# Optimization experiments

Measured on AMD Instinct MI355X. Metric: run time of the kernel, lower is better.

The kernel has to match this reference:

```python
import jax, jax.numpy as jnp
import numpy as np

EMB = 384
H = 6
D = 64  # head_size = EMB // H
FF = 4 * EMB
B, T = 256, 256
EPS = 1e-5


def layernorm(x, g, b):
    mu = jnp.mean(x, axis=-1, keepdims=True)
    var = jnp.var(x, axis=-1, keepdims=True)
    return (x - mu) * jax.lax.rsqrt(var + EPS) * g + b


def setup_inputs() -> dict:
    key = jax.random.key(0)
    ks = jax.random.split(key, 12)
    s_qkv = 1.0 / np.sqrt(EMB)
    return {
        "x":  jax.random.normal(ks[0], (B, T, EMB), jnp.float32),
        # per-head Q/K/V projections stacked: [EMB, H, D]
        "Wq": jax.random.normal(ks[1], (EMB, H, D), jnp.float32) * s_qkv,
        "Wk": jax.random.normal(ks[2], (EMB, H, D), jnp.float32) * s_qkv,
        "Wv": jax.random.normal(ks[3], (EMB, H, D), jnp.float32) * s_qkv,
        "Wo": jax.random.normal(ks[4], (EMB, EMB), jnp.float32) * s_qkv,
        "bo": jnp.zeros((EMB,), jnp.float32),
        "W1": jax.random.normal(ks[5], (EMB, FF), jnp.float32) * s_qkv,
        "b1": jnp.zeros((FF,), jnp.float32),
        "W2": jax.random.normal(ks[6], (FF, EMB), jnp.float32) * (1.0 / np.sqrt(FF)),
        "b2": jnp.zeros((EMB,), jnp.float32),
        "g1": jnp.ones((EMB,), jnp.float32),
        "be1": jnp.zeros((EMB,), jnp.float32),
        "g2": jnp.ones((EMB,), jnp.float32),
        "be2": jnp.zeros((EMB,), jnp.float32),
    }


def reference(x, Wq, Wk, Wv, Wo, bo, W1, b1, W2, b2, g1, be1, g2, be2):
    # pre-LN attention (unmasked encoder block, dropout in eval mode = identity)
    h = layernorm(x, g1, be1)                      # [B,T,C]
    q = jnp.einsum('btc,chd->bhtd', h, Wq)
    k = jnp.einsum('btc,chd->bhtd', h, Wk)
    v = jnp.einsum('btc,chd->bhtd', h, Wv)
    scores = jnp.einsum('bhtd,bhsd->bhts', q, k) * (D ** -0.5)
    attn = jax.nn.softmax(scores, axis=-1)         # [B,H,T,T]
    o = jnp.einsum('bhts,bhsd->bhtd', attn, v)
    o = o.transpose(0, 2, 1, 3).reshape(x.shape[0], x.shape[1], EMB)  # concat heads
    x = x + o @ Wo + bo
    h2 = layernorm(x, g2, be2)
    ff = jax.nn.relu(h2 @ W1 + b1) @ W2 + b2
    return x + ff
```

## Files before the change

### kernel.cpp

```cpp
#include <hip/hip_runtime.h>

typedef __attribute__((ext_vector_type(8))) short bf16x8;
typedef __attribute__((ext_vector_type(4))) float f32x4;
typedef __attribute__((ext_vector_type(4))) unsigned short u16x4;

#define DEVFN static __device__ __forceinline__

DEVFN unsigned short f2b(float f) {
  union { float f; unsigned u; } x; x.f = f;
  unsigned r = x.u + 0x7FFFu + ((x.u >> 16) & 1u);
  return (unsigned short)(r >> 16);
}

DEVFN void gll16(const void* g, void* l) {
  __builtin_amdgcn_global_load_lds(
      (const __attribute__((address_space(1))) unsigned int*)g,
      (__attribute__((address_space(3))) unsigned int*)l, 16, 0, 0);
}

#define MFMA16(a, b, c) __builtin_amdgcn_mfma_f32_16x16x32_bf16((a), (b), (c), 0, 0, 0)

__global__ __launch_bounds__(256) void prep_kernel(
    const float* __restrict__ Wq, const float* __restrict__ Wk, const float* __restrict__ Wv,
    const float* __restrict__ Wo, const float* __restrict__ W1, const float* __restrict__ W2,
    short* __restrict__ wqkvT, short* __restrict__ woT,
    short* __restrict__ w1T, short* __restrict__ w2T)
{
  int idx = blockIdx.x * 256 + threadIdx.x;
  if (idx < 442368) {
    int n = idx / 384, kk = idx - n * 384;
    int sec = n / 384, ww = n - sec * 384;
    const float* s = sec == 0 ? Wq : (sec == 1 ? Wk : Wv);
    wqkvT[idx] = (short)f2b(s[kk * 384 + ww]);
  } else if (idx < 589824) {
    int j = idx - 442368;
    int n = j / 384, kk = j - n * 384;
    woT[j] = (short)f2b(Wo[kk * 384 + n]);
  } else if (idx < 1179648) {
    int j = idx - 589824;
    int n = j / 384, kk = j - n * 384;
    w1T[j] = (short)f2b(W1[kk * 1536 + n]);
  } else if (idx < 1769472) {
    int j = idx - 1179648;
    int n = j / 1536, kk = j - n * 1536;
    w2T[j] = (short)f2b(W2[kk * 384 + n]);
  }
}

__global__ __launch_bounds__(256) void ln_kernel(
    const float* __restrict__ x, const float* __restrict__ g, const float* __restrict__ b,
    short* __restrict__ out)
{
  int row = blockIdx.x * 4 + (threadIdx.x >> 6);
  int l = threadIdx.x & 63;
  const float* xr = x + (size_t)row * 384;
  float v[6], s = 0.f, s2 = 0.f;
  #pragma unroll
  for (int i = 0; i < 6; ++i) { v[i] = xr[l + 64 * i]; s += v[i]; s2 += v[i] * v[i]; }
  #pragma unroll
  for (int m = 1; m < 64; m <<= 1) { s += __shfl_xor(s, m); s2 += __shfl_xor(s2, m); }
  float mu = s * (1.f / 384.f);
  float rs = rsqrtf(s2 * (1.f / 384.f) - mu * mu + 1e-5f);
  short* orow = out + (size_t)row * 384;
  #pragma unroll
  for (int i = 0; i < 6; ++i) {
    int c = l + 64 * i;
    orow[c] = (short)f2b((v[i] - mu) * rs * g[c] + b[c]);
  }
}

template<int EPI>
__global__ __launch_bounds__(512) void gemm_bt(
    const short* __restrict__ A, const short* __restrict__ BT,
    int K, int kt, int N, int nx,
    const float* __restrict__ bias, const float* __restrict__ resid,
    float* __restrict__ fout, short* __restrict__ bout,
    short* __restrict__ qb, short* __restrict__ kb, short* __restrict__ vb)
{
  __shared__ short As[256 * 64];
  __shared__ short Bs[128 * 64];
  const int tid = threadIdx.x;
  const int l = tid & 63, w = tid >> 6;
  const int cl = l & 15, rq = l >> 4;
  const int wr = (w >> 1) * 64, wc = (w & 1) * 64;

  const int nwg = gridDim.x, bid = blockIdx.x;
  const int q8 = nwg >> 3, r8 = nwg & 7;
  const int xcd = bid & 7, ii = bid >> 3;
  const int wg = (xcd < r8) ? xcd * (q8 + 1) + ii : r8 * (q8 + 1) + (xcd - r8) * q8 + ii;
  const int bx = wg % nx, by = wg / nx;

  const int m0 = by * 256, n0 = bx * 128;
  const short* Ab = A + (size_t)m0 * K;
  const short* Bb = BT + (size_t)n0 * K;

  f32x4 acc[4][4] = {};

  for (int ks = 0; ks < kt; ++ks) {
    const int k0 = ks * 64;
    __syncthreads();
    #pragma unroll
    for (int i = 0; i < 4; ++i) {
      int slot = i * 512 + tid;
      int row = slot >> 3, g = slot & 7;
      int gs = g ^ (row & 7);
      gll16(Ab + (size_t)row * K + k0 + gs * 8, &As[slot * 8]);
    }
    #pragma unroll
    for (int i = 0; i < 2; ++i) {
      int slot = i * 512 + tid;
      int row = slot >> 3, g = slot & 7;
      int gs = g ^ (row & 7);
      gll16(Bb + (size_t)row * K + k0 + gs * 8, &Bs[slot * 8]);
    }
    __syncthreads();
    #pragma unroll
    for (int kk = 0; kk < 2; ++kk) {
      bf16x8 af[4], bfr[4];
      #pragma unroll
      for (int m = 0; m < 4; ++m) {
        int row = wr + m * 16 + cl;
        af[m] = *(const bf16x8*)&As[row * 64 + (((kk * 4 + rq) ^ (row & 7)) * 8)];
      }
      #pragma unroll
      for (int n = 0; n < 4; ++n) {
        int row = wc + n * 16 + cl;
        bfr[n] = *(const bf16x8*)&Bs[row * 64 + (((kk * 4 + rq) ^ (row & 7)) * 8)];
      }
      #pragma unroll
      for (int m = 0; m < 4; ++m)
        #pragma unroll
        for (int n = 0; n < 4; ++n)
          acc[m][n] = MFMA16(af[m], bfr[n], acc[m][n]);
    }
  }

  const int gr0 = m0 + wr, gc0 = n0 + wc;
  #pragma unroll
  for (int m = 0; m < 4; ++m) {
    #pragma unroll
    for (int n = 0; n < 4; ++n) {
      int col = gc0 + n * 16 + cl;
      int rbase = gr0 + m * 16 + rq * 4;
      if constexpr (EPI == 0) {
        int sec = col / 384;
        int wcol = col - sec * 384;
        int hh = wcol >> 6, d = wcol & 63;
        int bidx = rbase >> 8, t0 = rbase & 255;
        if (sec == 2) {
          u16x4 pk;
          #pragma unroll
          for (int r = 0; r < 4; ++r) pk[r] = f2b(acc[m][n][r]);
          *(u16x4*)&vb[((size_t)(bidx * 6 + hh) * 64 + d) * 256 + t0] = pk;
        } else {
          short* dst = (sec == 0) ? qb : kb;
          float sc = (sec == 0) ? 0.125f : 1.0f;
          #pragma unroll
          for (int r = 0; r < 4; ++r)
            dst[((size_t)(bidx * 6 + hh) * 256 + t0 + r) * 64 + d] = (short)f2b(acc[m][n][r] * sc);
        }
      } else if constexpr (EPI == 1) {
        #pragma unroll
        for (int r = 0; r < 4; ++r) {
          size_t ix = (size_t)(rbase + r) * N + col;
          fout[ix] = acc[m][n][r] + bias[col] + resid[ix];
        }
      } else {
        #pragma unroll
        for (int r = 0; r < 4; ++r)
          bout[(size_t)(rbase + r) * N + col] = (short)f2b(fmaxf(acc[m][n][r] + bias[col], 0.f));
      }
    }
  }
}

__global__ __launch_bounds__(256) void attn_kernel(
    const short* __restrict__ qg, const short* __restrict__ kg,
    const short* __restrict__ vg, short* __restrict__ og)
{
  __shared__ short Ks[256 * 64];
  __shared__ short Vs[64 * 256];
  __shared__ float Pb[4][16 * 36];
  const int tid = threadIdx.x;
  const int bh = blockIdx.x >> 2;
  const int q0 = (blockIdx.x & 3) * 64;
  const int w = tid >> 6, l = tid & 63;
  const int cl = l & 15, rq = l >> 4;
  const short* kgb = kg + (size_t)bh * 16384;
  const short* vgb = vg + (size_t)bh * 16384;
  #pragma unroll
  for (int i = 0; i < 8; ++i) {
    int slot = i * 256 + tid;
    int row = slot >> 3, g = slot & 7;
    gll16(kgb + row * 64 + (g ^ (row & 7)) * 8, &Ks[slot * 8]);
  }
  #pragma unroll
  for (int i = 0; i < 8; ++i) {
    int slot = i * 256 + tid;
    int row = slot >> 5, g = slot & 31;
    int gs = (g & 24) | ((g ^ row) & 7);
    gll16(vgb + row * 256 + gs * 8, &Vs[slot * 8]);
  }
  const int qrow = q0 + w * 16 + cl;
  const bf16x8* qp = (const bf16x8*)(qg + ((size_t)bh * 256 + qrow) * 64 + rq * 8);
  bf16x8 qf0 = qp[0];
  bf16x8 qf1 = qp[4];
  __syncthreads();

  f32x4 s[16] = {};
  #pragma unroll
  for (int c = 0; c < 16; ++c) {
    int scol = c * 16 + cl;
    bf16x8 b0 = *(const bf16x8*)&Ks[scol * 64 + ((rq ^ (scol & 7)) * 8)];
    bf16x8 b1 = *(const bf16x8*)&Ks[scol * 64 + (((4 + rq) ^ (scol & 7)) * 8)];
    s[c] = MFMA16(qf0, b0, s[c]);
    s[c] = MFMA16(qf1, b1, s[c]);
  }
  float mx[4], inv[4];
  #pragma unroll
  for (int r = 0; r < 4; ++r) {
    float m = s[0][r];
    #pragma unroll
    for (int c = 1; c < 16; ++c) m = fmaxf(m, s[c][r]);
    #pragma unroll
    for (int msk = 1; msk < 16; msk <<= 1) m = fmaxf(m, __shfl_xor(m, msk));
    mx[r] = m;
  }
  #pragma unroll
  for (int r = 0; r < 4; ++r) {
    float t = 0.f;
    #pragma unroll
    for (int c = 0; c < 16; ++c) { float e = __expf(s[c][r] - mx[r]); s[c][r] = e; t += e; }
    #pragma unroll
    for (int msk = 1; msk < 16; msk <<= 1) t += __shfl_xor(t, msk);
    inv[r] = 1.f / t;
  }
  #pragma unroll
  for (int c = 0; c < 16; ++c) {
    #pragma unroll
    for (int r = 0; r < 4; ++r) s[c][r] *= inv[r];
  }
  f32x4 oacc[4] = {};
  float* Pw = Pb[w];
  #pragma unroll
  for (int ch = 0; ch < 8; ++ch) {
    #pragma unroll
    for (int r = 0; r < 4; ++r) {
      Pw[(4 * rq + r) * 36 + cl]      = s[2 * ch][r];
      Pw[(4 * rq + r) * 36 + 16 + cl] = s[2 * ch + 1][r];
    }
    f32x4 lo = *(const f32x4*)&Pw[cl * 36 + rq * 8];
    f32x4 hi = *(const f32x4*)&Pw[cl * 36 + rq * 8 + 4];
    bf16x8 pa;
    #pragma unroll
    for (int j = 0; j < 4; ++j) { pa[j] = (short)f2b(lo[j]); pa[j + 4] = (short)f2b(hi[j]); }
    #pragma unroll
    for (int n = 0; n < 4; ++n) {
      int vrow = n * 16 + cl;
      int gg = ch * 4 + rq;
      int gs = (gg & 24) | ((gg ^ vrow) & 7);
      bf16x8 vf = *(const bf16x8*)&Vs[vrow * 256 + gs * 8];
      oacc[n] = MFMA16(pa, vf, oacc[n]);
    }
  }
  int b = bh / 6, hh = bh - b * 6;
  #pragma unroll
  for (int n = 0; n < 4; ++n) {
    #pragma unroll
    for (int r = 0; r < 4; ++r) {
      int trow = q0 + w * 16 + 4 * rq + r;
      og[((size_t)(b * 256 + trow)) * 384 + hh * 64 + n * 16 + cl] = (short)f2b(oacc[n][r]);
    }
  }
}

extern "C" void kernel_launch(void* const* d_in, const int* in_sizes, int n_in,
                              void* d_out, int out_size, void* d_ws, size_t ws_size,
                              hipStream_t stream) {
  const float* x   = (const float*)d_in[0];
  const float* Wq  = (const float*)d_in[1];
  const float* Wk  = (const float*)d_in[2];
  const float* Wv  = (const float*)d_in[3];
  const float* Wo  = (const float*)d_in[4];
  const float* bo  = (const float*)d_in[5];
  const float* W1  = (const float*)d_in[6];
  const float* b1  = (const float*)d_in[7];
  const float* W2  = (const float*)d_in[8];
  const float* b2  = (const float*)d_in[9];
  const float* g1  = (const float*)d_in[10];
  const float* be1 = (const float*)d_in[11];
  const float* g2  = (const float*)d_in[12];
  const float* be2 = (const float*)d_in[13];

  char* ws = (char*)d_ws;
  short* wqkvT = (short*)(ws);
  short* woT   = (short*)(ws + 884736);
  short* w1T   = (short*)(ws + 1179648);
  short* w2T   = (short*)(ws + 2359296);
  short* bufA  = (short*)(ws + 3538944);
  short* h  = bufA;
  short* q  = bufA + 25165824;
  short* k  = bufA + 50331648;
  short* v  = bufA + 75497472;
  short* o  = bufA;
  short* h2 = bufA + 25165824;
  short* act = bufA + 50331648;
  float* out = (float*)d_out;

  prep_kernel<<<6912, 256, 0, stream>>>(Wq, Wk, Wv, Wo, W1, W2, wqkvT, woT, w1T, w2T);
  ln_kernel<<<16384, 256, 0, stream>>>(x, g1, be1, h);
  gemm_bt<0><<<9 * 256, 512, 0, stream>>>(h, wqkvT, 384, 6, 1152, 9,
      nullptr, nullptr, nullptr, nullptr, q, k, v);
  attn_kernel<<<6144, 256, 0, stream>>>(q, k, v, o);
  gemm_bt<1><<<3 * 256, 512, 0, stream>>>(o, woT, 384, 6, 384, 3,
      bo, x, out, nullptr, nullptr, nullptr, nullptr);
  ln_kernel<<<16384, 256, 0, stream>>>(out, g2, be2, h2);
  for (int c = 0; c < 2; ++c) {
    const size_t roff = (size_t)c * 32768 * 384;
    const size_t ooff = (size_t)c * 32768 * 384;
    gemm_bt<2><<<12 * 128, 512, 0, stream>>>(h2 + roff, w1T, 384, 6, 1536, 12,
        b1, nullptr, nullptr, act, nullptr, nullptr, nullptr);
    gemm_bt<1><<<3 * 128, 512, 0, stream>>>(act, w2T, 1536, 24, 384, 3,
        b2, out + ooff, out + ooff, nullptr, nullptr, nullptr, nullptr);
  }
}
```

Before: 528.9 us.

## Process full head per 1024-thread attention block with register-level P transpose

Each attention block now covers one whole (batch, head) with 16 waves instead of a quarter of it, so K and V are staged into LDS once per head rather than four times. The score MFMA swaps its operands so each lane holds one query's scores, which shrinks the softmax reductions to two cross-lane shuffles. P is converted to bf16 with the packed convert instruction and redistributed via ds_bpermute instead of an LDS round trip. Normalization is deferred to the output write. The trade-offs are larger blocks that may limit occupancy and scheduling flexibility.

Result: faster. 514.0 us (-2.8%).

```diff
diff --git a/kernel.cpp b/kernel.cpp
--- a/kernel.cpp
+++ b/kernel.cpp
@@ -3,6 +3,7 @@
 typedef __attribute__((ext_vector_type(8))) short bf16x8;
 typedef __attribute__((ext_vector_type(4))) float f32x4;
 typedef __attribute__((ext_vector_type(4))) unsigned short u16x4;
+typedef __attribute__((ext_vector_type(4))) unsigned int u32x4;
 
 #define DEVFN static __device__ __forceinline__
 
@@ -10,6 +11,12 @@
   union { float f; unsigned u; } x; x.f = f;
   unsigned r = x.u + 0x7FFFu + ((x.u >> 16) & 1u);
   return (unsigned short)(r >> 16);
+}
+
+DEVFN unsigned cvtpk(float lo, float hi) {
+  unsigned r;
+  asm("v_cvt_pk_bf16_f32 %0, %1, %2" : "=v"(r) : "v"(lo), "v"(hi));
+  return r;
 }
 
 DEVFN void gll16(const void* g, void* l) {
@@ -174,86 +181,92 @@
   }
 }
 
-__global__ __launch_bounds__(256) void attn_kernel(
+__global__ __launch_bounds__(1024) void attn_kernel(
     const short* __restrict__ qg, const short* __restrict__ kg,
     const short* __restrict__ vg, short* __restrict__ og)
 {
   __shared__ short Ks[256 * 64];
   __shared__ short Vs[64 * 256];
-  __shared__ float Pb[4][16 * 36];
   const int tid = threadIdx.x;
-  const int bh = blockIdx.x >> 2;
-  const int q0 = (blockIdx.x & 3) * 64;
+  const int bh = blockIdx.x;
   const int w = tid >> 6, l = tid & 63;
   const int cl = l & 15, rq = l >> 4;
   const short* kgb = kg + (size_t)bh * 16384;
   const short* vgb = vg + (size_t)bh * 16384;
   #pragma unroll
-  for (int i = 0; i < 8; ++i) {
-    int slot = i * 256 + tid;
+  for (int i = 0; i < 2; ++i) {
+    int slot = i * 1024 + tid;
     int row = slot >> 3, g = slot & 7;
     gll16(kgb + row * 64 + (g ^ (row & 7)) * 8, &Ks[slot * 8]);
   }
   #pragma unroll
-  for (int i = 0; i < 8; ++i) {
-    int slot = i * 256 + tid;
+  for (int i = 0; i < 2; ++i) {
+    int slot = i * 1024 + tid;
     int row = slot >> 5, g = slot & 31;
     int gs = (g & 24) | ((g ^ row) & 7);
     gll16(vgb + row * 256 + gs * 8, &Vs[slot * 8]);
   }
-  const int qrow = q0 + w * 16 + cl;
+  const int qrow = w * 16 + cl;
   const bf16x8* qp = (const bf16x8*)(qg + ((size_t)bh * 256 + qrow) * 64 + rq * 8);
-  bf16x8 qf0 = qp[0];
-  bf16x8 qf1 = qp[4];
+  bf16x8 qf0 = qp[0], qf1 = qp[4];
+  const int b = bh / 6, hh = bh - b * 6;
   __syncthreads();
 
   f32x4 s[16] = {};
   #pragma unroll
   for (int c = 0; c < 16; ++c) {
-    int scol = c * 16 + cl;
-    bf16x8 b0 = *(const bf16x8*)&Ks[scol * 64 + ((rq ^ (scol & 7)) * 8)];
-    bf16x8 b1 = *(const bf16x8*)&Ks[scol * 64 + (((4 + rq) ^ (scol & 7)) * 8)];
-    s[c] = MFMA16(qf0, b0, s[c]);
-    s[c] = MFMA16(qf1, b1, s[c]);
-  }
-  float mx[4], inv[4];
-  #pragma unroll
-  for (int r = 0; r < 4; ++r) {
-    float m = s[0][r];
-    #pragma unroll
-    for (int c = 1; c < 16; ++c) m = fmaxf(m, s[c][r]);
-    #pragma unroll
-    for (int msk = 1; msk < 16; msk <<= 1) m = fmaxf(m, __shfl_xor(m, msk));
-    mx[r] = m;
-  }
-  #pragma unroll
-  for (int r = 0; r < 4; ++r) {
-    float t = 0.f;
-    #pragma unroll
-    for (int c = 0; c < 16; ++c) { float e = __expf(s[c][r] - mx[r]); s[c][r] = e; t += e; }
-    #pragma unroll
-    for (int msk = 1; msk < 16; msk <<= 1) t += __shfl_xor(t, msk);
-    inv[r] = 1.f / t;
-  }
+    int srow = c * 16 + cl;
+    bf16x8 k0 = *(const bf16x8*)&Ks[srow * 64 + ((rq ^ (srow & 7)) * 8)];
+    bf16x8 k1 = *(const bf16x8*)&Ks[srow * 64 + (((4 + rq) ^ (srow & 7)) * 8)];
+    s[c] = MFMA16(k0, qf0, s[c]);
+    s[c] = MFMA16(k1, qf1, s[c]);
+  }
+  float mr[8];
+  #pragma unroll
+  for (int c = 0; c < 8; ++c)
+    mr[c] = fmaxf(fmaxf(fmaxf(s[2*c][0], s[2*c][1]), fmaxf(s[2*c][2], s[2*c][3])),
+                  fmaxf(fmaxf(s[2*c+1][0], s[2*c+1][1]), fmaxf(s[2*c+1][2], s[2*c+1][3])));
+  float m = fmaxf(fmaxf(fmaxf(mr[0], mr[1]), fmaxf(mr[2], mr[3])),
+                  fmaxf(fmaxf(mr[4], mr[5]), fmaxf(mr[6], mr[7])));
+  m = fmaxf(m, __shfl_xor(m, 16));
+  m = fmaxf(m, __shfl_xor(m, 32));
+  float tc[16];
   #pragma unroll
   for (int c = 0; c < 16; ++c) {
     #pragma unroll
-    for (int r = 0; r < 4; ++r) s[c][r] *= inv[r];
-  }
+    for (int r = 0; r < 4; ++r) s[c][r] = __expf(s[c][r] - m);
+    tc[c] = (s[c][0] + s[c][1]) + (s[c][2] + s[c][3]);
+  }
+  float t = ((tc[0]+tc[1])+(tc[2]+tc[3])) + ((tc[4]+tc[5])+(tc[6]+tc[7]))
+          + ((tc[8]+tc[9])+(tc[10]+tc[11])) + ((tc[12]+tc[13])+(tc[14]+tc[15]));
+  t += __shfl_xor(t, 16);
+  t += __shfl_xor(t, 32);
+  const float inv = 1.f / t;
+
   f32x4 oacc[4] = {};
-  float* Pw = Pb[w];
+  const int idx1 = (((2 * rq) & 3) * 16 + cl) << 2;
+  const int idx2 = (((2 * rq + 1) & 3) * 16 + cl) << 2;
+  const bool up = rq >= 2;
   #pragma unroll
   for (int ch = 0; ch < 8; ++ch) {
-    #pragma unroll
-    for (int r = 0; r < 4; ++r) {
-      Pw[(4 * rq + r) * 36 + cl]      = s[2 * ch][r];
-      Pw[(4 * rq + r) * 36 + 16 + cl] = s[2 * ch + 1][r];
-    }
-    f32x4 lo = *(const f32x4*)&Pw[cl * 36 + rq * 8];
-    f32x4 hi = *(const f32x4*)&Pw[cl * 36 + rq * 8 + 4];
-    bf16x8 pa;
-    #pragma unroll
-    for (int j = 0; j < 4; ++j) { pa[j] = (short)f2b(lo[j]); pa[j + 4] = (short)f2b(hi[j]); }
+    int X0 = (int)cvtpk(s[2*ch][0], s[2*ch][1]);
+    int X1 = (int)cvtpk(s[2*ch][2], s[2*ch][3]);
+    int X2 = (int)cvtpk(s[2*ch+1][0], s[2*ch+1][1]);
+    int X3 = (int)cvtpk(s[2*ch+1][2], s[2*ch+1][3]);
+    int lo0 = __builtin_amdgcn_ds_bpermute(idx1, X0);
+    int lo1 = __builtin_amdgcn_ds_bpermute(idx1, X1);
+    int hi0 = __builtin_amdgcn_ds_bpermute(idx1, X2);
+    int hi1 = __builtin_amdgcn_ds_bpermute(idx1, X3);
+    int lo2 = __builtin_amdgcn_ds_bpermute(idx2, X0);
+    int lo3 = __builtin_amdgcn_ds_bpermute(idx2, X1);
+    int hi2 = __builtin_amdgcn_ds_bpermute(idx2, X2);
+    int hi3 = __builtin_amdgcn_ds_bpermute(idx2, X3);
+    u32x4 words;
+    words[0] = (unsigned)(up ? hi0 : lo0);
+    words[1] = (unsigned)(up ? hi1 : lo1);
+    words[2] = (unsigned)(up ? hi2 : lo2);
+    words[3] = (unsigned)(up ? hi3 : lo3);
+    bf16x8 pa = __builtin_bit_cast(bf16x8, words);
     #pragma unroll
     for (int n = 0; n < 4; ++n) {
       int vrow = n * 16 + cl;
@@ -263,13 +276,16 @@
       oacc[n] = MFMA16(pa, vf, oacc[n]);
     }
   }
-  int b = bh / 6, hh = bh - b * 6;
+  float invr[4];
+  #pragma unroll
+  for (int r = 0; r < 4; ++r) invr[r] = __shfl(inv, 4 * rq + r);
   #pragma unroll
   for (int n = 0; n < 4; ++n) {
     #pragma unroll
     for (int r = 0; r < 4; ++r) {
-      int trow = q0 + w * 16 + 4 * rq + r;
-      og[((size_t)(b * 256 + trow)) * 384 + hh * 64 + n * 16 + cl] = (short)f2b(oacc[n][r]);
+      int trow = w * 16 + 4 * rq + r;
+      og[((size_t)(b * 256 + trow)) * 384 + hh * 64 + n * 16 + cl] =
+          (short)f2b(oacc[n][r] * invr[r]);
     }
   }
 }
@@ -311,7 +327,7 @@
   ln_kernel<<<16384, 256, 0, stream>>>(x, g1, be1, h);
   gemm_bt<0><<<9 * 256, 512, 0, stream>>>(h, wqkvT, 384, 6, 1152, 9,
       nullptr, nullptr, nullptr, nullptr, q, k, v);
-  attn_kernel<<<6144, 256, 0, stream>>>(q, k, v, o);
+  attn_kernel<<<1536, 1024, 0, stream>>>(q, k, v, o);
   gemm_bt<1><<<3 * 256, 512, 0, stream>>>(o, woT, 384, 6, 384, 3,
       bo, x, out, nullptr, nullptr, nullptr, nullptr);
   ln_kernel<<<16384, 256, 0, stream>>>(out, g2, be2, h2);
```
